# Kernel tuning notes

Measured on AMD Instinct MI355X. Metric: run time of the kernel, lower is better.

The kernel has to match this reference:

```python
import jax, jax.numpy as jnp
import numpy as np

B, C, H, W = 2, 128, 64, 64
EPS = 1e-5


def setup_inputs() -> dict:
    key = jax.random.key(0)
    ks = jax.random.split(key, 8)
    sc = 1.0 / np.sqrt(C)
    inp = {
        "x": jax.random.normal(ks[0], (B, C, H, W, 2), jnp.float32),
        # naive complex BN affine params: per-channel, per-component (real/imag)
        "bn_w": jnp.ones((C, 2), jnp.float32),
        "bn_b": jnp.zeros((C, 2), jnp.float32),
        # complex 1x1 conv weights: (out_c, in_c, 2) -> [..,0]=W_real, [..,1]=W_imag
        "wq": jax.random.normal(ks[1], (C, C, 2), jnp.float32) * sc,
        "bq": jnp.zeros((C, 2), jnp.float32),
        "wk": jax.random.normal(ks[2], (C, C, 2), jnp.float32) * sc,
        "bk": jnp.zeros((C, 2), jnp.float32),
        "wv": jax.random.normal(ks[3], (C, C, 2), jnp.float32) * sc,
        "bv": jnp.zeros((C, 2), jnp.float32),
        "gamma": jnp.float32(0.05),
    }
    return inp


def _complex_bn(x, w, b):
    # naive complex BN: normalize real and imag independently per channel
    # x: (B,C,H,W,2); stats over (B,H,W) per (C, component)
    mean = x.mean(axis=(0, 2, 3), keepdims=True)
    var = x.var(axis=(0, 2, 3), keepdims=True)
    xn = (x - mean) * jax.lax.rsqrt(var + EPS)
    return xn * w[None, :, None, None, :] + b[None, :, None, None, :]


def _complex_conv1x1(x, w, b):
    # x: (B,C,H,W,2); w: (O,C,2); b: (O,2)
    xr, xi = x[..., 0], x[..., 1]
    wr, wi = w[..., 0], w[..., 1]
    yr = jnp.einsum('oc,bchw->bohw', wr, xr) - jnp.einsum('oc,bchw->bohw', wi, xi)
    yi = jnp.einsum('oc,bchw->bohw', wr, xi) + jnp.einsum('oc,bchw->bohw', wi, xr)
    yr = yr + b[:, 0][None, :, None, None]
    yi = yi + b[:, 1][None, :, None, None]
    return jnp.stack([yr, yi], axis=-1)


def _attention(x, wq, bq, wk, bk, wv, bv, gamma):
    scale = C ** (-0.5)
    N = H * W
    # q,k,v: (B,C,H,W,2) -> (B,C,N,2) -> (B,N,C,2)
    to_tokens = lambda t: t.reshape(B, C, N, 2).transpose(0, 2, 1, 3)
    q = to_tokens(_complex_conv1x1(x, wq, bq))
    k = to_tokens(_complex_conv1x1(x, wk, bk))
    v = to_tokens(_complex_conv1x1(x, wv, bv))

    qr, qi = q[..., 0], q[..., 1]          # (B,N,C)
    kr, ki = k[..., 0], -k[..., 1]         # conjugate of k
    # k_t = conj(k) with token/channel axes swapped -> (B,C,N)
    ktr = kr.transpose(0, 2, 1)
    kti = ki.transpose(0, 2, 1)

    # complex matmul q @ k_t -> only the real part is used downstream
    attn_real = jnp.einsum('bnc,bcm->bnm', qr, ktr) - jnp.einsum('bnc,bcm->bnm', qi, kti)
    attn_w = jax.nn.softmax(attn_real * scale, axis=-1)  # (B,N,N)
    # dropout = identity (eval mode)

    # attn is purely real -> complex matmul reduces to two real matmuls
    out_r = jnp.einsum('bnm,bmc->bnc', attn_w, v[..., 0])
    out_i = jnp.einsum('bnm,bmc->bnc', attn_w, v[..., 1])
    out = jnp.stack([out_r, out_i], axis=-1)              # (B,N,C,2)
    out = out.transpose(0, 2, 1, 3).reshape(B, C, H, W, 2)
    return x + gamma * out


def reference(x, bn_w, bn_b, wq, bq, wk, bk, wv, bv, gamma):
    xn = _complex_bn(x, bn_w, bn_b)
    return _attention(xn, wq, bq, wk, bk, wv, bv, gamma)
```

## Files before the change

kernel.cpp:

```cpp
#include <hip/hip_runtime.h>
#include <hip/hip_bf16.h>
#include <hip/hip_fp8.h>

typedef __bf16 bf16_t;
typedef __bf16 bf16x8 __attribute__((ext_vector_type(8)));
typedef float  f32x4  __attribute__((ext_vector_type(4)));
typedef long   i64_t;

#define MFMA16(A,B,C) __builtin_amdgcn_mfma_f32_16x16x32_bf16((A),(B),(C),0,0,0)
#define MFMA8(A,B,C)  __builtin_amdgcn_mfma_f32_16x16x32_fp8_fp8((A),(B),(C),0,0,0)
#define MFMA85(A,B,C) __builtin_amdgcn_mfma_f32_16x16x32_bf8_fp8((A),(B),(C),0,0,0)

constexpr int Bn = 2, Cc = 128, Hh = 64, Wd = 64;
constexpr int N  = Hh * Wd;
constexpr int T  = Bn * N;
constexpr int D  = 2 * Cc;
constexpr int NSP = 4;
constexpr float EPS = 1e-5f;
constexpr float SCL = 0.08838834764831845f * 1.4426950408889634f;
constexpr float PSH = 9.0f;

__device__ __forceinline__ int tfrag(int row, int ch) {
    return (((ch >> 5) * 4 + (row >> 4)) << 10) +
           ((((ch >> 3) & 3) * 16 + (row & 15)) << 4) + (ch & 7) * 2;
}

__device__ __forceinline__ void gl16(const void* g, void* l) {
    __builtin_amdgcn_global_load_lds(
        (const __attribute__((address_space(1))) void*)g,
        (__attribute__((address_space(3))) void*)l, 16, 0, 0);
}

__global__ void k_pre(const float* __restrict__ x, float4* __restrict__ part,
                      const float* __restrict__ wq, const float* __restrict__ wk,
                      const float* __restrict__ wv, const float* __restrict__ bq,
                      const float* __restrict__ bk, const float* __restrict__ bv,
                      char* __restrict__ Wg, float* __restrict__ bt) {
    int tid = threadIdx.x;
    if (blockIdx.x < 512) {
        int bid = blockIdx.x;
        int q = bid >> 7, c = bid & 127;
        float sr = 0.f, si = 0.f, qr = 0.f, qi = 0.f;
        for (int b = 0; b < Bn; ++b) {
            const float4* p = (const float4*)((const float2*)x +
                              (size_t)(b * Cc + c) * N + q * 1024);
            for (int i = tid; i < 512; i += 256) {
                float4 v = p[i];
                sr += v.x + v.z; si += v.y + v.w;
                qr += v.x * v.x + v.z * v.z; qi += v.y * v.y + v.w * v.w;
            }
        }
        #pragma unroll
        for (int d = 32; d >= 1; d >>= 1) {
            sr += __shfl_xor(sr, d); si += __shfl_xor(si, d);
            qr += __shfl_xor(qr, d); qi += __shfl_xor(qi, d);
        }
        __shared__ float red[4][4];
        int w = tid >> 6;
        if ((tid & 63) == 0) { red[w][0] = sr; red[w][1] = si; red[w][2] = qr; red[w][3] = qi; }
        __syncthreads();
        if (tid == 0) {
            part[c * 4 + q] = make_float4(red[0][0] + red[1][0] + red[2][0] + red[3][0],
                                          red[0][1] + red[1][1] + red[2][1] + red[3][1],
                                          red[0][2] + red[1][2] + red[2][2] + red[3][2],
                                          red[0][3] + red[1][3] + red[2][3] + red[3][3]);
        }
    } else {
        int o = blockIdx.x - 512;
        int k = tid;
        int proj = o >> 8, oc = o & 255;
        const float* wsrc = proj == 0 ? wq : (proj == 1 ? wk : wv);
        const float* bsrc = proj == 0 ? bq : (proj == 1 ? bk : bv);
        int co = oc >> 7, oo = oc & 127;
        int c = k & 127, kc = k >> 7;
        float val;
        if (co == 0) val = (kc == 0) ? wsrc[(oo * 128 + c) * 2 + 0] : -wsrc[(oo * 128 + c) * 2 + 1];
        else         val = (kc == 0) ? wsrc[(oo * 128 + c) * 2 + 1] :  wsrc[(oo * 128 + c) * 2 + 0];
        int tile = o >> 6, row = o & 63;
        *(bf16_t*)(Wg + (size_t)tile * 32768 + tfrag(row, k)) = (bf16_t)val;
        if (k == 0) bt[o] = bsrc[oo * 2 + co];
    }
}

__global__ void k_norm(const float* __restrict__ x, const float4* __restrict__ part,
                       const float* __restrict__ bn_w, const float* __restrict__ bn_b,
                       char* __restrict__ XNg) {
    __shared__ float4 ssl[128];
    __shared__ __align__(16) char Tsh[32768];
    int blk = blockIdx.x;
    int b = blk >> 6, hw0 = (blk & 63) * 64;
    int tid = threadIdx.x;
    if (tid < 128) {
        float4 p0 = part[tid * 4 + 0], p1 = part[tid * 4 + 1];
        float4 p2 = part[tid * 4 + 2], p3 = part[tid * 4 + 3];
        float sr = p0.x + p1.x + p2.x + p3.x, si = p0.y + p1.y + p2.y + p3.y;
        float qr = p0.z + p1.z + p2.z + p3.z, qi = p0.w + p1.w + p2.w + p3.w;
        const float inv = 1.0f / (float)(Bn * N);
        float mr = sr * inv, mi = si * inv;
        float vr = qr * inv - mr * mr, vi = qi * inv - mi * mi;
        float scr = bn_w[tid * 2 + 0] * rsqrtf(vr + EPS);
        float sci = bn_w[tid * 2 + 1] * rsqrtf(vi + EPS);
        ssl[tid] = make_float4(scr, bn_b[tid * 2 + 0] - mr * scr,
                               sci, bn_b[tid * 2 + 1] - mi * sci);
    }
    __syncthreads();
    const float4* xin4 = (const float4*)x;
    #pragma unroll
    for (int it = 0; it < 16; ++it) {
        int idx = it * 256 + tid;
        int c = idx >> 5, h2 = (idx & 31) * 2;
        size_t gi = ((size_t)(b * Cc + c) * N + hw0 + h2) >> 1;
        float4 v = xin4[gi];
        float4 s = ssl[c];
        *(bf16_t*)(Tsh + tfrag(h2, c))           = (bf16_t)(v.x * s.x + s.y);
        *(bf16_t*)(Tsh + tfrag(h2, c + 128))     = (bf16_t)(v.y * s.z + s.w);
        *(bf16_t*)(Tsh + tfrag(h2 + 1, c))       = (bf16_t)(v.z * s.x + s.y);
        *(bf16_t*)(Tsh + tfrag(h2 + 1, c + 128)) = (bf16_t)(v.w * s.z + s.w);
    }
    __syncthreads();
    #pragma unroll
    for (int it = 0; it < 8; ++it) {
        int idx = it * 256 + tid;
        *(uint4*)(XNg + (size_t)blk * 32768 + idx * 16) = *(const uint4*)(Tsh + idx * 16);
    }
}

__global__ __launch_bounds__(256) void k_qkv(const char* __restrict__ XNg,
        const char* __restrict__ Wg, const float* __restrict__ bt,
        char* __restrict__ Qg, char* __restrict__ Kg, char* __restrict__ Vg) {
    __shared__ __align__(16) char Xsh[32768];
    __shared__ __align__(16) char Wsh[32768];
    int mx = blockIdx.x, ny = blockIdx.y;
    int tid = threadIdx.x;
    int w = tid >> 6, lane = tid & 63, n15 = lane & 15, quad = lane >> 4;
    const char* xs = XNg + (size_t)mx * 32768;
    const char* wsp = Wg + (size_t)ny * 32768;
    #pragma unroll
    for (int i = 0; i < 8; ++i) {
        int off = (w * 8 + i) * 1024 + lane * 16;
        gl16(xs + off, Xsh + off);
        gl16(wsp + off, Wsh + off);
    }
    __syncthreads();
    f32x4 acc[4] = {};
    #pragma unroll
    for (int ks = 0; ks < 8; ++ks) {
        bf16x8 a = *(const bf16x8*)(Xsh + (ks * 4 + w) * 1024 + lane * 16);
        #pragma unroll
        for (int t = 0; t < 4; ++t) {
            bf16x8 bw = *(const bf16x8*)(Wsh + (ks * 4 + t) * 1024 + lane * 16);
            acc[t] = MFMA16(a, bw, acc[t]);
        }
    }
    int proj = ny >> 2;
    int jb = (ny & 3) * 64;
    __syncthreads();
    char* Osh = Xsh;
    #pragma unroll
    for (int t = 0; t < 4; ++t) {
        float bias = bt[ny * 64 + t * 16 + n15];
        unsigned w01 = (unsigned)__builtin_amdgcn_cvt_pk_fp8_f32(
            acc[t][0] + bias, acc[t][1] + bias, 0, false);
        unsigned w23 = (unsigned)__builtin_amdgcn_cvt_pk_fp8_f32(
            acc[t][2] + bias, acc[t][3] + bias, 0, false);
        unsigned char vb[4] = {(unsigned char)(w01 & 0xff), (unsigned char)((w01 >> 8) & 0xff),
                               (unsigned char)(w23 & 0xff), (unsigned char)((w23 >> 8) & 0xff)};
        #pragma unroll
        for (int r = 0; r < 4; ++r) {
            if (proj < 2) {
                int lf  = (t >> 1) * 4 + w;
                int lif = (((2 * t + (n15 >> 3)) & 3) << 4) + quad * 4 + r;
                Osh[lf * 512 + lif * 8 + (n15 & 7)] = vb[r];
            } else {
                int key = w * 16 + quad * 4 + r;
                int lf  = (w >> 1) * 4 + t;
                int lif = (((key >> 3) & 3) << 4) + n15;
                Osh[lf * 512 + lif * 8 + (key & 7)] = vb[r];
            }
        }
    }
    __syncthreads();
    {
        int lf = tid >> 5, sub = (tid & 31) * 16;
        size_t tile = (proj == 0) ? (size_t)mx
                                  : (size_t)((mx >> 6) * 64 + (mx & 63));
        int gfrag = (proj < 2) ? ((jb >> 5) * 4 + lf)
                               : ((lf >> 2) * 16 + (jb >> 4) + (lf & 3));
        char* dst = (proj == 0 ? Qg : (proj == 1 ? Kg : Vg));
        *(uint4*)(dst + tile * 16384 + (size_t)gfrag * 512 + sub) =
            *(const uint4*)(Osh + tid * 16);
    }
}

__global__ __launch_bounds__(256, 4) void k_attn(const char* __restrict__ Qg,
        const char* __restrict__ Kg, const char* __restrict__ Vg,
        bf16_t* __restrict__ Opb, float* __restrict__ Lp) {
    __shared__ __align__(16) char Ksh[16384];
    __shared__ __align__(16) char Vsh[16384];
    __shared__ __align__(16) char Psh[4096];
    int bid = blockIdx.x;
    int grp = bid & 7, qt = bid >> 3;
    int sp = grp & 3, b = grp >> 2;
    int tid = threadIdx.x;
    int w = tid >> 6, lane = tid & 63, n15 = lane & 15, quad = lane >> 4;
    int r = w >> 1, h = w & 1;

    const i64_t ONES = 0x3838383838383838L;

    i64_t qf[2][8];
    const char* qb = Qg + (size_t)(b * 64 + qt) * 16384;
    #pragma unroll
    for (int g = 0; g < 2; ++g)
        #pragma unroll
        for (int ks = 0; ks < 8; ++ks)
            qf[g][ks] = *(const i64_t*)(qb + ((ks * 4 + r * 2 + g) << 9) + lane * 8);

    f32x4 o[2][8] = {};
    f32x4 l_[2] = {};

    for (int kt = 0; kt < 16; ++kt) {
        size_t tb = (size_t)(b * 64 + sp * 16 + kt) * 16384;
        __syncthreads();
        #pragma unroll
        for (int i = 0; i < 4; ++i) {
            int off = (w * 4 + i) * 1024 + lane * 16;
            gl16(Kg + tb + off, Ksh + off);
            gl16(Vg + tb + off, Vsh + off);
        }
        __syncthreads();

        f32x4 s[2][2] = {};
        #pragma unroll
        for (int ks = 0; ks < 8; ++ks) {
            #pragma unroll
            for (int c = 0; c < 2; ++c) {
                i64_t kf = *(const i64_t*)(Ksh + ((ks * 4 + h * 2 + c) << 9) + lane * 8);
                s[0][c] = MFMA8(qf[0][ks], kf, s[0][c]);
                s[1][c] = MFMA8(qf[1][ks], kf, s[1][c]);
            }
        }
        #pragma unroll
        for (int g = 0; g < 2; ++g)
            #pragma unroll
            for (int c = 0; c < 2; ++c) {
                float p0 = __builtin_amdgcn_exp2f(s[g][c][0] * SCL - PSH);
                float p1 = __builtin_amdgcn_exp2f(s[g][c][1] * SCL - PSH);
                float p2 = __builtin_amdgcn_exp2f(s[g][c][2] * SCL - PSH);
                float p3 = __builtin_amdgcn_exp2f(s[g][c][3] * SCL - PSH);
                unsigned w01 = (unsigned)__builtin_amdgcn_cvt_pk_bf8_f32(p0, p1, 0, false);
                unsigned w23 = (unsigned)__builtin_amdgcn_cvt_pk_bf8_f32(p2, p3, 0, false);
                char* pb = Psh + ((h * 4 + r * 2 + g) << 9) +
                           (((c * 2 + (n15 >> 3)) * 16 + quad * 4) << 3) + (n15 & 7);
                pb[0]  = (unsigned char)(w01 & 0xff);
                pb[8]  = (unsigned char)((w01 >> 8) & 0xff);
                pb[16] = (unsigned char)(w23 & 0xff);
                pb[24] = (unsigned char)((w23 >> 8) & 0xff);
            }
        __syncthreads();

        #pragma unroll
        for (int k2 = 0; k2 < 2; ++k2) {
            i64_t pa0 = *(const i64_t*)(Psh + ((k2 * 4 + r * 2 + 0) << 9) + lane * 8);
            i64_t pa1 = *(const i64_t*)(Psh + ((k2 * 4 + r * 2 + 1) << 9) + lane * 8);
            l_[0] = MFMA85(pa0, ONES, l_[0]);
            l_[1] = MFMA85(pa1, ONES, l_[1]);
            #pragma unroll
            for (int ct = 0; ct < 8; ++ct) {
                i64_t vf = *(const i64_t*)(Vsh + ((k2 * 16 + h * 8 + ct) << 9) + lane * 8);
                o[0][ct] = MFMA85(pa0, vf, o[0][ct]);
                o[1][ct] = MFMA85(pa1, vf, o[1][ct]);
            }
        }
    }
    int tok0 = b * N + qt * 64 + r * 32;
    #pragma unroll
    for (int g = 0; g < 2; ++g) {
        #pragma unroll
        for (int ct = 0; ct < 8; ++ct)
            #pragma unroll
            for (int ri = 0; ri < 4; ++ri)
                Opb[((size_t)sp * T + tok0 + g * 16 + quad * 4 + ri) * D +
                    h * 128 + ct * 16 + n15] = (bf16_t)o[g][ct][ri];
        if (h == 0 && n15 == 0) {
            #pragma unroll
            for (int ri = 0; ri < 4; ++ri)
                Lp[sp * T + tok0 + g * 16 + quad * 4 + ri] = l_[g][ri];
        }
    }
}

__global__ void k_comb(const bf16_t* __restrict__ Opb, const float* __restrict__ Lp,
                       const float4* __restrict__ part, const float* __restrict__ bn_w,
                       const float* __restrict__ bn_b, const float* __restrict__ x,
                       const float* __restrict__ gamma, float* __restrict__ out) {
    __shared__ float4 ssl[128];
    __shared__ float wts[16];
    __shared__ float Ot[256 * 17];
    int blk = blockIdx.x;
    int b = blk >> 8, hw0 = (blk & 255) * 16;
    int tok0 = b * N + hw0;
    int tid = threadIdx.x;
    if (tid < 128) {
        float4 p0 = part[tid * 4 + 0], p1 = part[tid * 4 + 1];
        float4 p2 = part[tid * 4 + 2], p3 = part[tid * 4 + 3];
        float sr = p0.x + p1.x + p2.x + p3.x, si = p0.y + p1.y + p2.y + p3.y;
        float qr = p0.z + p1.z + p2.z + p3.z, qi = p0.w + p1.w + p2.w + p3.w;
        const float inv = 1.0f / (float)(Bn * N);
        float mr = sr * inv, mi = si * inv;
        float vr = qr * inv - mr * mr, vi = qi * inv - mi * mi;
        float scr = bn_w[tid * 2 + 0] * rsqrtf(vr + EPS);
        float sci = bn_w[tid * 2 + 1] * rsqrtf(vi + EPS);
        ssl[tid] = make_float4(scr, bn_b[tid * 2 + 0] - mr * scr,
                               sci, bn_b[tid * 2 + 1] - mi * sci);
    }
    if (tid < 16) {
        float Z = 0.f;
        #pragma unroll
        for (int s = 0; s < NSP; ++s) Z += Lp[s * T + tok0 + tid];
        wts[tid] = gamma[0] / Z;
    }
    __syncthreads();
    #pragma unroll
    for (int i = 0; i < 2; ++i) {
        int idx = i * 256 + tid;
        int tk = idx >> 5, chunk = idx & 31;
        size_t base = (size_t)(tok0 + tk) * D + chunk * 8;
        float acc[8] = {};
        #pragma unroll
        for (int s = 0; s < NSP; ++s) {
            bf16x8 v = *(const bf16x8*)(Opb + (size_t)s * T * D + base);
            #pragma unroll
            for (int j = 0; j < 8; ++j) acc[j] += (float)v[j];
        }
        float ww = wts[tk];
        #pragma unroll
        for (int j = 0; j < 8; ++j) Ot[(chunk * 8 + j) * 17 + tk] = acc[j] * ww;
    }
    __syncthreads();
    const float2* xin = (const float2*)x;
    float2* xo = (float2*)out;
    #pragma unroll
    for (int i = 0; i < 8; ++i) {
        int linear = i * 256 + tid;
        int c = linear >> 4, hwo = linear & 15;
        size_t idx = (size_t)(b * Cc + c) * N + hw0 + hwo;
        float2 v = xin[idx];
        float4 s = ssl[c];
        float2 res;
        res.x = v.x * s.x + s.y + Ot[c * 17 + hwo];
        res.y = v.y * s.z + s.w + Ot[(128 + c) * 17 + hwo];
        xo[idx] = res;
    }
}

extern "C" void kernel_launch(void* const* d_in, const int* in_sizes, int n_in,
                              void* d_out, int out_size, void* d_ws, size_t ws_size,
                              hipStream_t stream) {
    const float* x    = (const float*)d_in[0];
    const float* bn_w = (const float*)d_in[1];
    const float* bn_b = (const float*)d_in[2];
    const float* wq   = (const float*)d_in[3];
    const float* bq   = (const float*)d_in[4];
    const float* wk   = (const float*)d_in[5];
    const float* bk   = (const float*)d_in[6];
    const float* wv   = (const float*)d_in[7];
    const float* bv   = (const float*)d_in[8];
    const float* gam  = (const float*)d_in[9];
    float* out = (float*)d_out;

    char* ws = (char*)d_ws;
    size_t off = 0;
    auto alloc = [&](size_t bytes) -> void* {
        void* p = ws + off;
        off += (bytes + 255) & ~(size_t)255;
        return p;
    };
    float4* part = (float4*)alloc(512 * sizeof(float4));
    char*   XNg  = (char*)alloc((size_t)128 * 32768);
    char*   Wg   = (char*)alloc((size_t)12 * 32768);
    float*  bt   = (float*)alloc(768 * 4);
    char*   Qg   = (char*)alloc((size_t)128 * 16384);
    char*   Kg   = (char*)alloc((size_t)128 * 16384);
    char*   Vg   = (char*)alloc((size_t)128 * 16384);
    bf16_t* Opb  = (bf16_t*)alloc((size_t)NSP * T * D * 2);
    float*  Lp   = (float*)alloc((size_t)NSP * T * 4);

    k_pre<<<1280, 256, 0, stream>>>(x, part, wq, wk, wv, bq, bk, bv, Wg, bt);
    k_norm<<<128, 256, 0, stream>>>(x, part, bn_w, bn_b, XNg);
    k_qkv<<<dim3(128, 12), 256, 0, stream>>>(XNg, Wg, bt, Qg, Kg, Vg);
    k_attn<<<512, 256, 0, stream>>>(Qg, Kg, Vg, Opb, Lp);
    k_comb<<<512, 256, 0, stream>>>(Opb, Lp, part, bn_w, bn_b, x, gam, out);
}
```

Measured before the change: 150.0 us.

## Double-buffer K/V tiles in LDS to prefetch the next tile during compute

The attention kernel now keeps two LDS buffers each for K and V. It issues the global-to-LDS loads for tile kt+1 before computing QK^T and PV on tile kt, and uses a single barrier plus a vmcnt wait per iteration instead of two __syncthreads around a blocking load. The goal is to hide global load latency behind MFMA work. In exchange, LDS use per block roughly doubles and the launch-bounds occupancy hint of 4 is dropped, so fewer blocks may be resident per CU. The projection tile index simplification is an equivalent expression.

```diff
diff --git a/kernel.cpp b/kernel.cpp
--- a/kernel.cpp
+++ b/kernel.cpp
@@ -182,8 +182,7 @@
     __syncthreads();
     {
         int lf = tid >> 5, sub = (tid & 31) * 16;
-        size_t tile = (proj == 0) ? (size_t)mx
-                                  : (size_t)((mx >> 6) * 64 + (mx & 63));
+        size_t tile = (size_t)mx;
         int gfrag = (proj < 2) ? ((jb >> 5) * 4 + lf)
                                : ((lf >> 2) * 16 + (jb >> 4) + (lf & 3));
         char* dst = (proj == 0 ? Qg : (proj == 1 ? Kg : Vg));
@@ -192,11 +191,11 @@
     }
 }
 
-__global__ __launch_bounds__(256, 4) void k_attn(const char* __restrict__ Qg,
+__global__ __launch_bounds__(256) void k_attn(const char* __restrict__ Qg,
         const char* __restrict__ Kg, const char* __restrict__ Vg,
         bf16_t* __restrict__ Opb, float* __restrict__ Lp) {
-    __shared__ __align__(16) char Ksh[16384];
-    __shared__ __align__(16) char Vsh[16384];
+    __shared__ __align__(16) char Ksh[2 * 16384];
+    __shared__ __align__(16) char Vsh[2 * 16384];
     __shared__ __align__(16) char Psh[4096];
     int bid = blockIdx.x;
     int grp = bid & 7, qt = bid >> 3;
@@ -218,23 +217,39 @@
     f32x4 o[2][8] = {};
     f32x4 l_[2] = {};
 
+    size_t kbase = (size_t)(b * 64 + sp * 16) * 16384;
+    #pragma unroll
+    for (int i = 0; i < 4; ++i) {
+        int off = (w * 4 + i) * 1024 + lane * 16;
+        gl16(Kg + kbase + off, Ksh + off);
+        gl16(Vg + kbase + off, Vsh + off);
+    }
+
     for (int kt = 0; kt < 16; ++kt) {
-        size_t tb = (size_t)(b * 64 + sp * 16 + kt) * 16384;
-        __syncthreads();
-        #pragma unroll
-        for (int i = 0; i < 4; ++i) {
-            int off = (w * 4 + i) * 1024 + lane * 16;
-            gl16(Kg + tb + off, Ksh + off);
-            gl16(Vg + tb + off, Vsh + off);
-        }
-        __syncthreads();
-
+        int cur = kt & 1;
+        asm volatile("s_waitcnt vmcnt(0)" ::: "memory");
+        __builtin_amdgcn_s_barrier();
+        __builtin_amdgcn_sched_barrier(0);
+
+        if (kt < 15) {
+            size_t tb = kbase + (size_t)(kt + 1) * 16384;
+            char* kb = Ksh + (cur ^ 1) * 16384;
+            char* vb = Vsh + (cur ^ 1) * 16384;
+            #pragma unroll
+            for (int i = 0; i < 4; ++i) {
+                int off = (w * 4 + i) * 1024 + lane * 16;
+                gl16(Kg + tb + off, kb + off);
+                gl16(Vg + tb + off, vb + off);
+            }
+        }
+
+        const char* kc = Ksh + cur * 16384;
         f32x4 s[2][2] = {};
         #pragma unroll
         for (int ks = 0; ks < 8; ++ks) {
             #pragma unroll
             for (int c = 0; c < 2; ++c) {
-                i64_t kf = *(const i64_t*)(Ksh + ((ks * 4 + h * 2 + c) << 9) + lane * 8);
+                i64_t kf = *(const i64_t*)(kc + ((ks * 4 + h * 2 + c) << 9) + lane * 8);
                 s[0][c] = MFMA8(qf[0][ks], kf, s[0][c]);
                 s[1][c] = MFMA8(qf[1][ks], kf, s[1][c]);
             }
@@ -256,8 +271,11 @@
                 pb[16] = (unsigned char)(w23 & 0xff);
                 pb[24] = (unsigned char)((w23 >> 8) & 0xff);
             }
-        __syncthreads();
-
+        asm volatile("s_waitcnt lgkmcnt(0)" ::: "memory");
+        __builtin_amdgcn_s_barrier();
+        __builtin_amdgcn_sched_barrier(0);
+
+        const char* vc = Vsh + cur * 16384;
         #pragma unroll
         for (int k2 = 0; k2 < 2; ++k2) {
             i64_t pa0 = *(const i64_t*)(Psh + ((k2 * 4 + r * 2 + 0) << 9) + lane * 8);
@@ -266,7 +284,7 @@
             l_[1] = MFMA85(pa1, ONES, l_[1]);
             #pragma unroll
             for (int ct = 0; ct < 8; ++ct) {
-                i64_t vf = *(const i64_t*)(Vsh + ((k2 * 16 + h * 8 + ct) << 9) + lane * 8);
+                i64_t vf = *(const i64_t*)(vc + ((k2 * 16 + h * 8 + ct) << 9) + lane * 8);
                 o[0][ct] = MFMA85(pa0, vf, o[0][ct]);
                 o[1][ct] = MFMA85(pa1, vf, o[1][ct]);
             }
```

New measurement: 141.6 us. -5.6%, faster.
